# Kernel tuning notes

Hardware: AMD Instinct MI355X
Metric: run time of the kernel (lower is better)

The kernel has to match this reference:

```python
import jax, jax.numpy as jnp
import numpy as np

B, S, D, H, L, NITEMS = 512, 200, 64, 2, 2, 100000
HD = D // H
EPS = 1e-8
C = 0.001


def _ln(x, w, b):
    m = jnp.mean(x, -1, keepdims=True)
    v = jnp.mean((x - m) ** 2, -1, keepdims=True)
    return (x - m) / jnp.sqrt(v + EPS) * w + b


def _frob(x):
    return jnp.sqrt(jnp.sum(x * x))


def setup_inputs() -> dict:
    key = jax.random.key(0)
    ks = jax.random.split(key, 20)
    rn = lambda k, shape, s=0.02: jax.random.normal(k, shape, jnp.float32) * s
    item_emb = rn(ks[0], (NITEMS + 1, D))
    pos_emb = rn(ks[1], (S + 1, D)).at[0].set(0.0)  # padding_idx=0 row
    pred_w = rn(ks[2], (1, D))
    inp = {
        'user_ids': jax.random.randint(ks[3], (B,), 0, NITEMS, dtype=jnp.int32),
        'log_seqs': jax.random.randint(ks[4], (B, S), 0, NITEMS + 1, dtype=jnp.int32),
        'pos_seqs': jax.random.randint(ks[5], (B, S), 0, NITEMS + 1, dtype=jnp.int32),
        'item_emb': item_emb, 'pos_emb': pos_emb, 'pred_w': pred_w,
        'ln_w': jnp.ones((L, D), jnp.float32), 'ln_b': rn(ks[6], (L, D)),
        'qkv_w': rn(ks[7], (L, 3 * D, D)), 'qkv_b': rn(ks[8], (L, 3 * D)),
        'out_w': rn(ks[9], (L, D, D)), 'out_b': rn(ks[10], (L, D)),
        'fc1_w': rn(ks[11], (L, D, D)), 'fc1_b': rn(ks[12], (L, D)),
        'ffln_w': jnp.ones((L, D), jnp.float32), 'ffln_b': rn(ks[13], (L, D)),
        'fc2_w': rn(ks[14], (L, D, D)), 'fc2_b': rn(ks[15], (L, D)),
        'ffln2_w': jnp.ones((L, D), jnp.float32), 'ffln2_b': rn(ks[16], (L, D)),
    }
    return inp


def reference(user_ids, log_seqs, pos_seqs, item_emb, pos_emb, pred_w,
              ln_w, ln_b, qkv_w, qkv_b, out_w, out_b,
              fc1_w, fc1_b, ffln_w, ffln_b, fc2_w, fc2_b, ffln2_w, ffln2_b):
    # ---- log2feats ----
    x = item_emb[log_seqs] * jnp.sqrt(jnp.float32(D))  # (B,S,D)
    poss = jnp.arange(1, S + 1, dtype=log_seqs.dtype)[None, :] * (log_seqs != 0)
    x = x + pos_emb[poss]
    causal_bias = jnp.where(jnp.tril(jnp.ones((S, S), bool)), 0.0, -1e30).astype(jnp.float32)
    for l in range(L):
        q_in = _ln(x, ln_w[l], ln_b[l])  # query uses pre-LN, K/V use raw seqs
        q = (q_in @ qkv_w[l, :D].T + qkv_b[l, :D]).reshape(B, S, H, HD)
        k = (x @ qkv_w[l, D:2 * D].T + qkv_b[l, D:2 * D]).reshape(B, S, H, HD)
        v = (x @ qkv_w[l, 2 * D:].T + qkv_b[l, 2 * D:]).reshape(B, S, H, HD)
        sc = jnp.einsum('bqhd,bkhd->bhqk', q, k) / jnp.sqrt(jnp.float32(HD)) + causal_bias
        a = jax.nn.softmax(sc, -1)
        ctx = jnp.einsum('bhqk,bkhd->bqhd', a, v).reshape(B, S, D)
        x = q_in + ctx @ out_w[l].T + out_b[l]
        h = jax.nn.relu(_ln(x, ffln_w[l], ffln_b[l]) @ fc1_w[l].T + fc1_b[l])
        x = h @ fc2_w[l].T + fc2_b[l] + _ln(x, ffln2_w[l], ffln2_b[l])
    # ---- left(): quadratic form via Gram matrices (math identical to outer-product sum) ----
    FF = jnp.einsum('bsi,bsj->ij', x, x)          # sum_b F_b^T F_b  (d,d)
    EE = item_emb.T @ item_emb                      # (d,d)
    hh = pred_w.T @ pred_w                          # (d,d)
    left = C * jnp.sum(FF * EE * hh)
    # ---- right() ----
    ps = (x * item_emb[pos_seqs]) @ pred_w[0]       # (B,S), prediction has no bias
    right = jnp.sum((1.0 - C) * ps ** 2 - 2.0 * ps)
    # ---- reg_loss(): sum of per-parameter Frobenius norms ----
    reg = _frob(item_emb) + _frob(pos_emb) + _frob(pred_w)
    for p in (ln_w, ln_b, qkv_w, qkv_b, out_w, out_b, fc1_w, fc1_b,
              ffln_w, ffln_b, fc2_w, fc2_b, ffln2_w, ffln2_b):
        reg = reg + jnp.sum(jax.vmap(_frob)(p))  # per-layer params are separate tensors
    return left + right + 0.1 * reg
```

## Files before the change

### kernel.cpp

```cpp
#include <hip/hip_runtime.h>
#include <math.h>

#define BB 512
#define SS 200
#define DDIM 64
#define HD 32
#define LL 2
#define NROWS (BB * SS)
#define EPS 1e-8f
#define CC 0.001f
#define GRAM_NB 256
#define LSTRIDE 72
#define XS 68
#define QROWS 208

typedef __attribute__((ext_vector_type(8))) short bf16x8;
typedef __attribute__((ext_vector_type(4))) float f32x4;

__device__ unsigned short g_qb[NROWS * DDIM];
__device__ float g_gpart[2 * GRAM_NB * 4096];
__device__ unsigned short g_wb[49152];

__device__ __forceinline__ float wave_sum(float v) {
#pragma unroll
    for (int o = 32; o > 0; o >>= 1) v += __shfl_xor(v, o, 64);
    return v;
}
__device__ __forceinline__ unsigned short f2b(float f) {
    unsigned u = __float_as_uint(f);
    return (unsigned short)((u + 0x7FFFu + ((u >> 16) & 1u)) >> 16);
}

__global__ __launch_bounds__(256) void prep_weights(const float* __restrict__ qkv_w,
                                                    const float* __restrict__ out_w,
                                                    const float* __restrict__ fc1_w,
                                                    const float* __restrict__ fc2_w,
                                                    unsigned short* __restrict__ wb) {
    int i4 = (blockIdx.x * 256 + threadIdx.x) * 4;
    const float* src; int off;
    if (i4 < 24576)      { src = qkv_w; off = 0; }
    else if (i4 < 32768) { src = out_w; off = 24576; }
    else if (i4 < 40960) { src = fc1_w; off = 32768; }
    else                 { src = fc2_w; off = 40960; }
    float4 f = *(const float4*)&src[i4 - off];
    ushort4 o; o.x = f2b(f.x); o.y = f2b(f.y); o.z = f2b(f.z); o.w = f2b(f.w);
    *(ushort4*)&wb[i4] = o;
}

__device__ __forceinline__ bf16x8 frag_raw(const float* Xf, int row, int c0) {
    const float* p = &Xf[row * XS + c0];
    float4 u = *(const float4*)p;
    float4 v = *(const float4*)(p + 4);
    bf16x8 r;
    r[0] = (short)f2b(u.x); r[1] = (short)f2b(u.y); r[2] = (short)f2b(u.z); r[3] = (short)f2b(u.w);
    r[4] = (short)f2b(v.x); r[5] = (short)f2b(v.y); r[6] = (short)f2b(v.z); r[7] = (short)f2b(v.w);
    return r;
}
__device__ __forceinline__ bf16x8 frag_ln(const float* Xf, const float* stats,
                                          const float* vw, const float* vb,
                                          int row, int c0) {
    float m = stats[row * 2], rs = stats[row * 2 + 1];
    const float* p = &Xf[row * XS + c0];
    float4 u = *(const float4*)p;
    float4 v = *(const float4*)(p + 4);
    bf16x8 r;
    r[0] = (short)f2b((u.x - m) * rs * vw[c0 + 0] + vb[c0 + 0]);
    r[1] = (short)f2b((u.y - m) * rs * vw[c0 + 1] + vb[c0 + 1]);
    r[2] = (short)f2b((u.z - m) * rs * vw[c0 + 2] + vb[c0 + 2]);
    r[3] = (short)f2b((u.w - m) * rs * vw[c0 + 3] + vb[c0 + 3]);
    r[4] = (short)f2b((v.x - m) * rs * vw[c0 + 4] + vb[c0 + 4]);
    r[5] = (short)f2b((v.y - m) * rs * vw[c0 + 5] + vb[c0 + 5]);
    r[6] = (short)f2b((v.z - m) * rs * vw[c0 + 6] + vb[c0 + 6]);
    r[7] = (short)f2b((v.w - m) * rs * vw[c0 + 7] + vb[c0 + 7]);
    return r;
}

__device__ __forceinline__ void gemm_lds(bf16x8 a0, bf16x8 a1, const unsigned short* __restrict__ W,
                                         int m16, int quad, f32x4 acc[4]) {
#pragma unroll
    for (int nt = 0; nt < 4; ++nt) {
        bf16x8 b0 = *(const bf16x8*)&W[(nt * 16 + m16) * LSTRIDE + quad * 8];
        bf16x8 b1 = *(const bf16x8*)&W[(nt * 16 + m16) * LSTRIDE + 32 + quad * 8];
        acc[nt] = __builtin_amdgcn_mfma_f32_16x16x32_bf16(a0, b0, acc[nt], 0, 0, 0);
        acc[nt] = __builtin_amdgcn_mfma_f32_16x16x32_bf16(a1, b1, acc[nt], 0, 0, 0);
    }
}

__device__ __forceinline__ void stage_wb1024(const unsigned short* __restrict__ G,
                                             unsigned short* __restrict__ L, int t) {
    int r = t >> 4, c4 = (t & 15) * 4;
    *(ushort4*)&L[r * LSTRIDE + c4] = *(const ushort4*)&G[r * 64 + c4];
}

__global__ __launch_bounds__(1024)
void mega(const int* __restrict__ log_seqs,
          const int* __restrict__ pos_seqs,
          const float* __restrict__ item_emb,
          const float* __restrict__ pos_emb,
          const float* __restrict__ pred_w,
          const float* __restrict__ ln_w,  const float* __restrict__ ln_b,
          const float* __restrict__ qkv_b,
          const float* __restrict__ out_b,
          const float* __restrict__ fc1_b, const float* __restrict__ fc2_b,
          const float* __restrict__ ffln_w, const float* __restrict__ ffln_b,
          const float* __restrict__ ffln2_w, const float* __restrict__ ffln2_b,
          const unsigned short* __restrict__ wb,
          unsigned short* __restrict__ xb,
          float* __restrict__ rpart) {
    __shared__ float Xf[200 * XS];
    __shared__ unsigned short Qb[QROWS * 72];
    __shared__ unsigned short Kb[QROWS * 72];
    __shared__ unsigned short Vt[64 * 232];
    __shared__ unsigned short Wb[64 * LSTRIDE];
    __shared__ float stats[200 * 2];
    __shared__ float vecs[13][64];
    __shared__ float redw[16];

    const int t = threadIdx.x, b = blockIdx.x;
    const int w = t >> 6, lane = t & 63, m16 = lane & 15, quad = lane >> 4;
    const f32x4 Z = {0.f, 0.f, 0.f, 0.f};

    if (t < 64) vecs[12][t] = pred_w[t];
    if (t < 512) {
        int r2 = t >> 3, cc = 200 + (t & 7) * 4;
        ushort4 z4; z4.x = z4.y = z4.z = z4.w = 0;
        *(ushort4*)&Vt[r2 * 232 + cc] = z4;
    }
    {
        int rr = t >> 2;
        if (rr < 200) {
            int li = log_seqs[b * SS + rr];
            int poss = li ? (rr + 1) : 0;
            int qd = (t & 3) * 16;
            float4 v[4];
#pragma unroll
            for (int g = 0; g < 4; ++g) {
                float4 e = *(const float4*)&item_emb[(long)li * DDIM + qd + g * 4];
                float4 p = *(const float4*)&pos_emb[(long)poss * DDIM + qd + g * 4];
                v[g].x = e.x * 8.0f + p.x; v[g].y = e.y * 8.0f + p.y;
                v[g].z = e.z * 8.0f + p.z; v[g].w = e.w * 8.0f + p.w;
                *(float4*)&Xf[rr * XS + qd + g * 4] = v[g];
            }
            float s1 = 0.f, s2 = 0.f;
#pragma unroll
            for (int g = 0; g < 4; ++g) {
                s1 += (v[g].x + v[g].y) + (v[g].z + v[g].w);
                s2 += (v[g].x * v[g].x + v[g].y * v[g].y) + (v[g].z * v[g].z + v[g].w * v[g].w);
            }
            s1 += __shfl_xor(s1, 1, 64); s1 += __shfl_xor(s1, 2, 64);
            s2 += __shfl_xor(s2, 1, 64); s2 += __shfl_xor(s2, 2, 64);
            float mean = s1 * (1.f / 64.f);
            float var = s2 * (1.f / 64.f) - mean * mean;
            float rs = rsqrtf(var + EPS);
            if ((t & 3) == 0) { stats[rr * 2] = mean; stats[rr * 2 + 1] = rs; }
        }
    }
    __syncthreads();

    for (int l = 0; l < LL; ++l) {
        if (t < 64) {
            vecs[0][t] = qkv_b[l * 192 + t];
            vecs[1][t] = qkv_b[l * 192 + 64 + t];
            vecs[2][t] = qkv_b[l * 192 + 128 + t];
            vecs[3][t] = ln_w[l * 64 + t];   vecs[4][t] = ln_b[l * 64 + t];
            vecs[5][t] = out_b[l * 64 + t];
            vecs[6][t] = fc1_b[l * 64 + t];  vecs[7][t] = fc2_b[l * 64 + t];
            vecs[8][t] = ffln_w[l * 64 + t]; vecs[9][t] = ffln_b[l * 64 + t];
            vecs[10][t] = ffln2_w[l * 64 + t]; vecs[11][t] = ffln2_b[l * 64 + t];
        }
        stage_wb1024(wb + l * 12288, Wb, t);
        __syncthreads();
        if (w < 13) {
            int tb = w * 16;
            int row = tb + m16; if (row > 199) row = 199;
            bf16x8 a0 = frag_ln(Xf, stats, vecs[3], vecs[4], row, quad * 8);
            bf16x8 a1 = frag_ln(Xf, stats, vecs[3], vecs[4], row, 32 + quad * 8);
            f32x4 acc[4] = {Z, Z, Z, Z};
            gemm_lds(a0, a1, Wb, m16, quad, acc);
#pragma unroll
            for (int nt = 0; nt < 4; ++nt) {
                int n = nt * 16 + m16; float bbv = vecs[0][n];
#pragma unroll
                for (int rg = 0; rg < 4; ++rg)
                    Qb[(tb + quad * 4 + rg) * 72 + n] = f2b(acc[nt][rg] + bbv);
            }
        }
        __syncthreads();
        stage_wb1024(wb + l * 12288 + 4096, Wb, t);
        __syncthreads();
        if (w < 13) {
            int tb = w * 16;
            int row = tb + m16; if (row > 199) row = 199;
            bf16x8 a0 = frag_raw(Xf, row, quad * 8);
            bf16x8 a1 = frag_raw(Xf, row, 32 + quad * 8);
            f32x4 acc[4] = {Z, Z, Z, Z};
            gemm_lds(a0, a1, Wb, m16, quad, acc);
#pragma unroll
            for (int nt = 0; nt < 4; ++nt) {
                int n = nt * 16 + m16; float bbv = vecs[1][n];
#pragma unroll
                for (int rg = 0; rg < 4; ++rg)
                    Kb[(tb + quad * 4 + rg) * 72 + n] = f2b(acc[nt][rg] + bbv);
            }
        }
        __syncthreads();
        stage_wb1024(wb + l * 12288 + 8192, Wb, t);
        __syncthreads();
        if (w < 13) {
            int tb = w * 16;
            int row = tb + m16; if (row > 199) row = 199;
            bf16x8 a0 = frag_raw(Xf, row, quad * 8);
            bf16x8 a1 = frag_raw(Xf, row, 32 + quad * 8);
            f32x4 acc[4] = {Z, Z, Z, Z};
            gemm_lds(a0, a1, Wb, m16, quad, acc);
#pragma unroll
            for (int nt = 0; nt < 4; ++nt) {
                int n = nt * 16 + m16; float bbv = vecs[2][n];
#pragma unroll
                for (int rg = 0; rg < 4; ++rg) {
                    int m = tb + quad * 4 + rg;
                    if (m < 200) Vt[n * 232 + m] = f2b(acc[nt][rg] + bbv);
                }
            }
        }
        __syncthreads();
        {
            const unsigned long long tab0 = 0x01170016FF19FF18ull;
            const unsigned long long tab1 = 0x0513041203150214ull;
            const unsigned long long tab2 = 0x090F080E07110610ull;
            const unsigned long long tab3 = 0xFFFFFFFF0B0D0A0Cull;
            unsigned long long tv = (w & 8) ? ((w & 4) ? tab3 : tab2) : ((w & 4) ? tab1 : tab0);
            unsigned su = (unsigned)((tv >> ((w & 3) * 16)) & 0xFFFFu);
            const float scale = 0.17677669529663687f;
            for (int slot = 0; slot < 2; ++slot) {
                int u = (su >> (slot * 8)) & 0xFF;
                if (u == 0xFF) break;
                int h = u & 1, qt = u >> 1;
                int q0 = qt * 16;
                int qrow = q0 + m16; if (qrow > 199) qrow = 199;
                bf16x8 qa = *(const bf16x8*)&Qb[qrow * 72 + h * 32 + quad * 8];
                __builtin_amdgcn_wave_barrier();
                unsigned short* ps = &Qb[q0 * 72 + h * 32];
                f32x4 o0 = Z, o1 = Z;
                float lsum[4] = {0.f, 0.f, 0.f, 0.f};
                int np = (qt + 2) >> 1;
                for (int pi = 0; pi < np; ++pi) {
                    int p0 = pi * 32;
                    int kr0 = p0 + m16;      int kr0c = kr0 > 199 ? 199 : kr0;
                    int kr1 = p0 + 16 + m16; int kr1c = kr1 > 199 ? 199 : kr1;
                    bf16x8 kb0 = *(const bf16x8*)&Kb[kr0c * 72 + h * 32 + quad * 8];
                    bf16x8 kb1 = *(const bf16x8*)&Kb[kr1c * 72 + h * 32 + quad * 8];
                    f32x4 s0 = __builtin_amdgcn_mfma_f32_16x16x32_bf16(qa, kb0, Z, 0, 0, 0);
                    f32x4 s1 = __builtin_amdgcn_mfma_f32_16x16x32_bf16(qa, kb1, Z, 0, 0, 0);
                    float e0[4], e1[4];
#pragma unroll
                    for (int rg = 0; rg < 4; ++rg) {
                        int rglob = q0 + quad * 4 + rg;
                        e0[rg] = (kr0 <= rglob && kr0 < SS) ? __expf(s0[rg] * scale) : 0.f;
                        e1[rg] = (kr1 <= rglob && kr1 < SS) ? __expf(s1[rg] * scale) : 0.f;
                        lsum[rg] += e0[rg] + e1[rg];
                    }
                    __builtin_amdgcn_wave_barrier();
#pragma unroll
                    for (int rg = 0; rg < 4; ++rg) {
                        int row = quad * 4 + rg;
                        ps[row * 72 + m16] = f2b(e0[rg]);
                        ps[row * 72 + 16 + m16] = f2b(e1[rg]);
                    }
                    __builtin_amdgcn_wave_barrier();
                    bf16x8 pa = *(const bf16x8*)&ps[m16 * 72 + quad * 8];
                    bf16x8 vb0 = *(const bf16x8*)&Vt[(h * 32 + m16) * 232 + p0 + quad * 8];
                    bf16x8 vb1 = *(const bf16x8*)&Vt[(h * 32 + 16 + m16) * 232 + p0 + quad * 8];
                    o0 = __builtin_amdgcn_mfma_f32_16x16x32_bf16(pa, vb0, o0, 0, 0, 0);
                    o1 = __builtin_amdgcn_mfma_f32_16x16x32_bf16(pa, vb1, o1, 0, 0, 0);
                }
#pragma unroll
                for (int rg = 0; rg < 4; ++rg)
#pragma unroll
                    for (int o = 1; o <= 8; o <<= 1) lsum[rg] += __shfl_xor(lsum[rg], o, 64);
                __builtin_amdgcn_wave_barrier();
#pragma unroll
                for (int rg = 0; rg < 4; ++rg) {
                    int rglob = q0 + quad * 4 + rg;
                    if (rglob < SS) {
                        float inv = 1.f / lsum[rg];
                        Qb[rglob * 72 + h * 32 + m16] = f2b(o0[rg] * inv);
                        Qb[rglob * 72 + h * 32 + 16 + m16] = f2b(o1[rg] * inv);
                    }
                }
            }
        }
        __syncthreads();
        float core[4][4];
        stage_wb1024(wb + 24576 + l * 4096, Wb, t);
        __syncthreads();
        if (w < 13) {
            int tb = w * 16;
            int row = tb + m16; if (row > 199) row = 199;
            bf16x8 a0 = *(const bf16x8*)&Qb[row * 72 + quad * 8];
            bf16x8 a1 = *(const bf16x8*)&Qb[row * 72 + 32 + quad * 8];
            f32x4 acc1[4] = {Z, Z, Z, Z};
            gemm_lds(a0, a1, Wb, m16, quad, acc1);
#pragma unroll
            for (int nt = 0; nt < 4; ++nt) {
                int n = nt * 16 + m16;
                float bbv = vecs[5][n], lw = vecs[3][n], lb = vecs[4][n];
#pragma unroll
                for (int rg = 0; rg < 4; ++rg) {
                    int m = tb + quad * 4 + rg; int mc = m > 199 ? 199 : m;
                    float qin = (Xf[mc * XS + n] - stats[mc * 2]) * stats[mc * 2 + 1] * lw + lb;
                    core[nt][rg] = acc1[nt][rg] + bbv + qin;
                }
            }
#pragma unroll
            for (int rg = 0; rg < 4; ++rg) {
                float s1 = (core[0][rg] + core[1][rg]) + (core[2][rg] + core[3][rg]);
                float s2 = core[0][rg] * core[0][rg] + core[1][rg] * core[1][rg]
                         + core[2][rg] * core[2][rg] + core[3][rg] * core[3][rg];
#pragma unroll
                for (int o = 1; o <= 8; o <<= 1) { s1 += __shfl_xor(s1, o, 64); s2 += __shfl_xor(s2, o, 64); }
                float mean = s1 * (1.f / 64.f);
                float var = s2 * (1.f / 64.f) - mean * mean;
                float rs = rsqrtf(var + EPS);
#pragma unroll
                for (int nt = 0; nt < 4; ++nt) core[nt][rg] = (core[nt][rg] - mean) * rs;
            }
            __builtin_amdgcn_wave_barrier();
#pragma unroll
            for (int nt = 0; nt < 4; ++nt) {
                int n = nt * 16 + m16;
                float w8v = vecs[8][n], b9v = vecs[9][n];
#pragma unroll
                for (int rg = 0; rg < 4; ++rg)
                    Kb[(tb + quad * 4 + rg) * 72 + n] = f2b(core[nt][rg] * w8v + b9v);
            }
        }
        __syncthreads();
        stage_wb1024(wb + 32768 + l * 4096, Wb, t);
        __syncthreads();
        if (w < 13) {
            int tb = w * 16;
            bf16x8 a0 = *(const bf16x8*)&Kb[(tb + m16) * 72 + quad * 8];
            bf16x8 a1 = *(const bf16x8*)&Kb[(tb + m16) * 72 + 32 + quad * 8];
            f32x4 acc2[4] = {Z, Z, Z, Z};
            gemm_lds(a0, a1, Wb, m16, quad, acc2);
            __builtin_amdgcn_wave_barrier();
#pragma unroll
            for (int nt = 0; nt < 4; ++nt) {
                int n = nt * 16 + m16; float bbv = vecs[6][n];
#pragma unroll
                for (int rg = 0; rg < 4; ++rg)
                    Kb[(tb + quad * 4 + rg) * 72 + n] = f2b(fmaxf(acc2[nt][rg] + bbv, 0.f));
            }
        }
        __syncthreads();
        stage_wb1024(wb + 40960 + l * 4096, Wb, t);
        __syncthreads();
        if (w < 13) {
            int tb = w * 16;
            bf16x8 a0 = *(const bf16x8*)&Kb[(tb + m16) * 72 + quad * 8];
            bf16x8 a1 = *(const bf16x8*)&Kb[(tb + m16) * 72 + 32 + quad * 8];
            f32x4 acc3[4] = {Z, Z, Z, Z};
            gemm_lds(a0, a1, Wb, m16, quad, acc3);
            float xn[4][4];
#pragma unroll
            for (int nt = 0; nt < 4; ++nt) {
                int n = nt * 16 + m16;
                float bbv = vecs[7][n], lw = vecs[10][n], lb = vecs[11][n];
#pragma unroll
                for (int rg = 0; rg < 4; ++rg)
                    xn[nt][rg] = acc3[nt][rg] + bbv + core[nt][rg] * lw + lb;
            }
#pragma unroll
            for (int rg = 0; rg < 4; ++rg) {
                float s1 = (xn[0][rg] + xn[1][rg]) + (xn[2][rg] + xn[3][rg]);
                float s2 = xn[0][rg] * xn[0][rg] + xn[1][rg] * xn[1][rg]
                         + xn[2][rg] * xn[2][rg] + xn[3][rg] * xn[3][rg];
#pragma unroll
                for (int o = 1; o <= 8; o <<= 1) { s1 += __shfl_xor(s1, o, 64); s2 += __shfl_xor(s2, o, 64); }
                float mean = s1 * (1.f / 64.f);
                float var = s2 * (1.f / 64.f) - mean * mean;
                float rs = rsqrtf(var + EPS);
                int m = tb + quad * 4 + rg;
                if (m < 200) {
#pragma unroll
                    for (int nt = 0; nt < 4; ++nt) Xf[m * XS + nt * 16 + m16] = xn[nt][rg];
                    if (m16 == 0) { stats[m * 2] = mean; stats[m * 2 + 1] = rs; }
                }
            }
        }
        __syncthreads();
    }

    for (int i = t; i < 3200; i += 1024) {
        int r = i >> 4, c4 = (i & 15) * 4;
        float4 f = *(const float4*)&Xf[r * XS + c4];
        ushort4 o; o.x = f2b(f.x); o.y = f2b(f.y); o.z = f2b(f.z); o.w = f2b(f.w);
        *(ushort4*)&xb[((long)b * SS + r) * DDIM + c4] = o;
    }
    float local = 0.f;
    {
        int rr = t >> 2;
        if (rr < 200) {
            int pi = pos_seqs[b * SS + rr];
            int qd = (t & 3) * 16;
            float v = 0.f;
#pragma unroll
            for (int g = 0; g < 4; ++g) {
                float4 xv = *(const float4*)&Xf[rr * XS + qd + g * 4];
                float4 iv = *(const float4*)&item_emb[(long)pi * DDIM + qd + g * 4];
                const float* pwp = &vecs[12][qd + g * 4];
                v += xv.x * iv.x * pwp[0] + xv.y * iv.y * pwp[1]
                   + xv.z * iv.z * pwp[2] + xv.w * iv.w * pwp[3];
            }
            v += __shfl_xor(v, 1, 64); v += __shfl_xor(v, 2, 64);
            if ((t & 3) == 0) local += (1.0f - CC) * v * v - 2.0f * v;
        }
    }
    local = wave_sum(local);
    if (lane == 0) redw[w] = local;
    __syncthreads();
    if (t == 0) {
        float s = 0.f;
#pragma unroll
        for (int i = 0; i < 16; ++i) s += redw[i];
        rpart[b] = s;
    }
}

__global__ __launch_bounds__(256) void gram_kernel(const float* __restrict__ A0, int n0,
                                                   const unsigned short* __restrict__ A1, int n1,
                                                   float* __restrict__ part) {
    __shared__ unsigned short At[64 * LSTRIDE];
    int t = threadIdx.x;
    int second = blockIdx.x >= GRAM_NB;
    int bid = second ? blockIdx.x - GRAM_NB : blockIdx.x;
    int nrows = second ? n1 : n0;
    int w16 = (t >> 6) * 16, lane = t & 63, m16 = lane & 15, quad = lane >> 4;
    int bi = t & 15, bj = t >> 4;
    f32x4 zero = {0.f, 0.f, 0.f, 0.f};
    f32x4 acc[4] = {zero, zero, zero, zero};
    for (long base = (long)bid * 64; base < nrows; base += (long)GRAM_NB * 64) {
        __syncthreads();
        if (!second) {
            float rv[4][4];
#pragma unroll
            for (int e = 0; e < 4; ++e) {
                long gr = base + bj * 4 + e;
                float4 f = make_float4(0.f, 0.f, 0.f, 0.f);
                if (gr < nrows) f = *(const float4*)&A0[gr * DDIM + bi * 4];
                rv[e][0] = f.x; rv[e][1] = f.y; rv[e][2] = f.z; rv[e][3] = f.w;
            }
#pragma unroll
            for (int e = 0; e < 4; ++e) {
                ushort4 o;
                o.x = f2b(rv[0][e]); o.y = f2b(rv[1][e]); o.z = f2b(rv[2][e]); o.w = f2b(rv[3][e]);
                *(ushort4*)&At[(bi * 4 + e) * LSTRIDE + bj * 4] = o;
            }
        } else {
            ushort4 u[4];
#pragma unroll
            for (int e = 0; e < 4; ++e) {
                long gr = base + bj * 4 + e;
                ushort4 uu; uu.x = uu.y = uu.z = uu.w = 0;
                if (gr < nrows) uu = *(const ushort4*)&A1[gr * DDIM + bi * 4];
                u[e] = uu;
            }
#pragma unroll
            for (int e = 0; e < 4; ++e) {
                ushort4 o;
                o.x = ((const unsigned short*)&u[0])[e];
                o.y = ((const unsigned short*)&u[1])[e];
                o.z = ((const unsigned short*)&u[2])[e];
                o.w = ((const unsigned short*)&u[3])[e];
                *(ushort4*)&At[(bi * 4 + e) * LSTRIDE + bj * 4] = o;
            }
        }
        __syncthreads();
#pragma unroll
        for (int ks = 0; ks < 2; ++ks) {
            bf16x8 a = *(const bf16x8*)&At[(w16 + m16) * LSTRIDE + ks * 32 + quad * 8];
#pragma unroll
            for (int nt = 0; nt < 4; ++nt) {
                bf16x8 bfr = *(const bf16x8*)&At[(nt * 16 + m16) * LSTRIDE + ks * 32 + quad * 8];
                acc[nt] = __builtin_amdgcn_mfma_f32_16x16x32_bf16(a, bfr, acc[nt], 0, 0, 0);
            }
        }
    }
    float* slab = part + (long)blockIdx.x * 4096;
#pragma unroll
    for (int nt = 0; nt < 4; ++nt) {
        int n = nt * 16 + m16;
#pragma unroll
        for (int rg = 0; rg < 4; ++rg) {
            int m = w16 + quad * 4 + rg;
            slab[m * 64 + n] = acc[nt][rg];
        }
    }
}

struct NormEntry { const float* p; int n; };
struct NormArgs { NormEntry e[30]; };

__global__ __launch_bounds__(256) void reduce_norms(const float* __restrict__ part,
                                                    float* __restrict__ EE, float* __restrict__ FF,
                                                    NormArgs args, float* __restrict__ norms) {
    __shared__ float red[256];
    int blk = blockIdx.x;
    if (blk < 32) {
        int which = blk >> 4;
        int p = (blk & 15) * 256 + threadIdx.x;
        const float* basep = part + (long)which * GRAM_NB * 4096;
        float s = 0.f;
        for (int b = 0; b < GRAM_NB; ++b) s += basep[(long)b * 4096 + p];
        (which ? FF : EE)[p] = s;
    } else {
        NormEntry en = args.e[blk - 32];
        float s = 0.f;
        for (int i = threadIdx.x; i < en.n; i += 256) { float v = en.p[i]; s += v * v; }
        red[threadIdx.x] = s;
        for (int o = 128; o > 0; o >>= 1) {
            __syncthreads();
            if (threadIdx.x < o) red[threadIdx.x] += red[threadIdx.x + o];
        }
        __syncthreads();
        if (threadIdx.x == 0) norms[blk - 32] = red[0];
    }
}

__global__ __launch_bounds__(256) void final_kernel(const float* __restrict__ EE,
                                                    const float* __restrict__ FF,
                                                    const float* __restrict__ pred_w,
                                                    const float* __restrict__ rpart,
                                                    const float* __restrict__ norms,
                                                    float* __restrict__ out) {
    __shared__ float p_s[64];
    __shared__ float redL[256];
    __shared__ float redT[256];
    __shared__ float redR[256];
    int t = threadIdx.x;
    if (t < 64) p_s[t] = pred_w[t];
    __syncthreads();
    float lf = 0.f, tr = 0.f, rs = 0.f;
    for (int p = t; p < 4096; p += 256) {
        int i = p >> 6, j = p & 63;
        float ee = EE[p];
        lf += FF[p] * ee * p_s[i] * p_s[j];
        if (i == j) tr += ee;
    }
    for (int i = t; i < 512; i += 256) rs += rpart[i];
    redL[t] = lf; redT[t] = tr; redR[t] = rs;
    for (int o = 128; o > 0; o >>= 1) {
        __syncthreads();
        if (t < o) { redL[t] += redL[t + o]; redT[t] += redT[t + o]; redR[t] += redR[t + o]; }
    }
    __syncthreads();
    if (t == 0) {
        float reg = sqrtf(redT[0]);
        for (int s = 0; s < 30; ++s) reg += sqrtf(norms[s]);
        out[0] = CC * redL[0] + redR[0] + 0.1f * reg;
    }
}

struct DevPtrs { float* gpart; unsigned short *qb, *wb; };

static DevPtrs fetch_ptrs() {
    DevPtrs p;
    (void)hipGetSymbolAddress((void**)&p.gpart, HIP_SYMBOL(g_gpart));
    (void)hipGetSymbolAddress((void**)&p.qb,    HIP_SYMBOL(g_qb));
    (void)hipGetSymbolAddress((void**)&p.wb,    HIP_SYMBOL(g_wb));
    return p;
}

extern "C" void kernel_launch(void* const* d_in, const int* in_sizes, int n_in,
                              void* d_out, int out_size, void* d_ws, size_t ws_size,
                              hipStream_t stream) {
    const int*   log_seqs = (const int*)d_in[1];
    const int*   pos_seqs = (const int*)d_in[2];
    const float* item_emb = (const float*)d_in[3];
    const float* pos_emb  = (const float*)d_in[4];
    const float* pred_w   = (const float*)d_in[5];
    const float* ln_w     = (const float*)d_in[6];
    const float* ln_b     = (const float*)d_in[7];
    const float* qkv_w    = (const float*)d_in[8];
    const float* qkv_b    = (const float*)d_in[9];
    const float* out_w    = (const float*)d_in[10];
    const float* out_b    = (const float*)d_in[11];
    const float* fc1_w    = (const float*)d_in[12];
    const float* fc1_b    = (const float*)d_in[13];
    const float* ffln_w   = (const float*)d_in[14];
    const float* ffln_b   = (const float*)d_in[15];
    const float* fc2_w    = (const float*)d_in[16];
    const float* fc2_b    = (const float*)d_in[17];
    const float* ffln2_w  = (const float*)d_in[18];
    const float* ffln2_b  = (const float*)d_in[19];

    static DevPtrs P = fetch_ptrs();

    float* ws    = (float*)d_ws;
    float* rpart = ws;
    float* nrm   = ws + 1664;
    float* EE    = ws + 2048;
    float* FF    = ws + 6144;

    prep_weights<<<48, 256, 0, stream>>>(qkv_w, out_w, fc1_w, fc2_w, P.wb);

    mega<<<BB, 1024, 0, stream>>>(log_seqs, pos_seqs, item_emb, pos_emb, pred_w,
                                  ln_w, ln_b, qkv_b, out_b, fc1_b, fc2_b,
                                  ffln_w, ffln_b, ffln2_w, ffln2_b,
                                  P.wb, P.qb, rpart);

    gram_kernel<<<2 * GRAM_NB, 256, 0, stream>>>(item_emb, 100001, P.qb, NROWS, P.gpart);

    NormArgs na;
    int s = 0;
    na.e[s++] = {pos_emb, (SS + 1) * DDIM};
    na.e[s++] = {pred_w, DDIM};
    for (int l = 0; l < LL; ++l) {
        na.e[s++] = {ln_w + l * 64, 64};
        na.e[s++] = {ln_b + l * 64, 64};
        na.e[s++] = {qkv_w + (long)l * 12288, 12288};
        na.e[s++] = {qkv_b + (long)l * 192, 192};
        na.e[s++] = {out_w + (long)l * 4096, 4096};
        na.e[s++] = {out_b + l * 64, 64};
        na.e[s++] = {fc1_w + (long)l * 4096, 4096};
        na.e[s++] = {fc1_b + l * 64, 64};
        na.e[s++] = {ffln_w + l * 64, 64};
        na.e[s++] = {ffln_b + l * 64, 64};
        na.e[s++] = {fc2_w + (long)l * 4096, 4096};
        na.e[s++] = {fc2_b + l * 64, 64};
        na.e[s++] = {ffln2_w + l * 64, 64};
        na.e[s++] = {ffln2_b + l * 64, 64};
    }
    reduce_norms<<<62, 256, 0, stream>>>(P.gpart, EE, FF, na, nrm);

    final_kernel<<<1, 256, 0, stream>>>(EE, FF, pred_w, rpart, nrm, (float*)d_out);
}
```

Baseline: 241.2 us.

## Drop weight-prep and final kernels via in-kernel bf16 conversion and last-block reduction

Removes the separate prep_weights launch by converting fp32 weights to bf16 while staging them into LDS inside the main kernel. It also merges reduce_norms and final_kernel into one launch, where the last block to arrive (tracked by an atomic counter that the main kernel resets) computes the final scalar. Two accumulator arrays are reused in place to reduce register pressure. The aim is to cut launch overhead, at the cost of redundant fp32 loads and conversions in every block plus a fence-and-atomic handshake.

```diff
diff --git a/kernel.cpp b/kernel.cpp
--- a/kernel.cpp
+++ b/kernel.cpp
@@ -19,7 +19,6 @@
 
 __device__ unsigned short g_qb[NROWS * DDIM];
 __device__ float g_gpart[2 * GRAM_NB * 4096];
-__device__ unsigned short g_wb[49152];
 
 __device__ __forceinline__ float wave_sum(float v) {
 #pragma unroll
@@ -29,22 +28,6 @@
 __device__ __forceinline__ unsigned short f2b(float f) {
     unsigned u = __float_as_uint(f);
     return (unsigned short)((u + 0x7FFFu + ((u >> 16) & 1u)) >> 16);
-}
-
-__global__ __launch_bounds__(256) void prep_weights(const float* __restrict__ qkv_w,
-                                                    const float* __restrict__ out_w,
-                                                    const float* __restrict__ fc1_w,
-                                                    const float* __restrict__ fc2_w,
-                                                    unsigned short* __restrict__ wb) {
-    int i4 = (blockIdx.x * 256 + threadIdx.x) * 4;
-    const float* src; int off;
-    if (i4 < 24576)      { src = qkv_w; off = 0; }
-    else if (i4 < 32768) { src = out_w; off = 24576; }
-    else if (i4 < 40960) { src = fc1_w; off = 32768; }
-    else                 { src = fc2_w; off = 40960; }
-    float4 f = *(const float4*)&src[i4 - off];
-    ushort4 o; o.x = f2b(f.x); o.y = f2b(f.y); o.z = f2b(f.z); o.w = f2b(f.w);
-    *(ushort4*)&wb[i4] = o;
 }
 
 __device__ __forceinline__ bf16x8 frag_raw(const float* Xf, int row, int c0) {
@@ -86,10 +69,12 @@
     }
 }
 
-__device__ __forceinline__ void stage_wb1024(const unsigned short* __restrict__ G,
-                                             unsigned short* __restrict__ L, int t) {
+__device__ __forceinline__ void stage_wf32(const float* __restrict__ G,
+                                           unsigned short* __restrict__ L, int t) {
     int r = t >> 4, c4 = (t & 15) * 4;
-    *(ushort4*)&L[r * LSTRIDE + c4] = *(const ushort4*)&G[r * 64 + c4];
+    float4 f = *(const float4*)&G[r * 64 + c4];
+    ushort4 o; o.x = f2b(f.x); o.y = f2b(f.y); o.z = f2b(f.z); o.w = f2b(f.w);
+    *(ushort4*)&L[r * LSTRIDE + c4] = o;
 }
 
 __global__ __launch_bounds__(1024)
@@ -104,9 +89,11 @@
           const float* __restrict__ fc1_b, const float* __restrict__ fc2_b,
           const float* __restrict__ ffln_w, const float* __restrict__ ffln_b,
           const float* __restrict__ ffln2_w, const float* __restrict__ ffln2_b,
-          const unsigned short* __restrict__ wb,
+          const float* __restrict__ qkv_w, const float* __restrict__ out_w,
+          const float* __restrict__ fc1_w, const float* __restrict__ fc2_w,
           unsigned short* __restrict__ xb,
-          float* __restrict__ rpart) {
+          float* __restrict__ rpart,
+          unsigned int* __restrict__ cnt) {
     __shared__ float Xf[200 * XS];
     __shared__ unsigned short Qb[QROWS * 72];
     __shared__ unsigned short Kb[QROWS * 72];
@@ -120,6 +107,7 @@
     const int w = t >> 6, lane = t & 63, m16 = lane & 15, quad = lane >> 4;
     const f32x4 Z = {0.f, 0.f, 0.f, 0.f};
 
+    if (b == 0 && t == 0) *cnt = 0u;
     if (t < 64) vecs[12][t] = pred_w[t];
     if (t < 512) {
         int r2 = t >> 3, cc = 200 + (t & 7) * 4;
@@ -168,7 +156,7 @@
             vecs[8][t] = ffln_w[l * 64 + t]; vecs[9][t] = ffln_b[l * 64 + t];
             vecs[10][t] = ffln2_w[l * 64 + t]; vecs[11][t] = ffln2_b[l * 64 + t];
         }
-        stage_wb1024(wb + l * 12288, Wb, t);
+        stage_wf32(qkv_w + l * 12288, Wb, t);
         __syncthreads();
         if (w < 13) {
             int tb = w * 16;
@@ -186,7 +174,7 @@
             }
         }
         __syncthreads();
-        stage_wb1024(wb + l * 12288 + 4096, Wb, t);
+        stage_wf32(qkv_w + l * 12288 + 4096, Wb, t);
         __syncthreads();
         if (w < 13) {
             int tb = w * 16;
@@ -204,7 +192,7 @@
             }
         }
         __syncthreads();
-        stage_wb1024(wb + l * 12288 + 8192, Wb, t);
+        stage_wf32(qkv_w + l * 12288 + 8192, Wb, t);
         __syncthreads();
         if (w < 13) {
             int tb = w * 16;
@@ -291,16 +279,16 @@
             }
         }
         __syncthreads();
-        float core[4][4];
-        stage_wb1024(wb + 24576 + l * 4096, Wb, t);
+        f32x4 core4[4];
+        stage_wf32(out_w + l * 4096, Wb, t);
         __syncthreads();
         if (w < 13) {
             int tb = w * 16;
             int row = tb + m16; if (row > 199) row = 199;
             bf16x8 a0 = *(const bf16x8*)&Qb[row * 72 + quad * 8];
             bf16x8 a1 = *(const bf16x8*)&Qb[row * 72 + 32 + quad * 8];
-            f32x4 acc1[4] = {Z, Z, Z, Z};
-            gemm_lds(a0, a1, Wb, m16, quad, acc1);
+            core4[0] = Z; core4[1] = Z; core4[2] = Z; core4[3] = Z;
+            gemm_lds(a0, a1, Wb, m16, quad, core4);
 #pragma unroll
             for (int nt = 0; nt < 4; ++nt) {
                 int n = nt * 16 + m16;
@@ -309,21 +297,21 @@
                 for (int rg = 0; rg < 4; ++rg) {
                     int m = tb + quad * 4 + rg; int mc = m > 199 ? 199 : m;
                     float qin = (Xf[mc * XS + n] - stats[mc * 2]) * stats[mc * 2 + 1] * lw + lb;
-                    core[nt][rg] = acc1[nt][rg] + bbv + qin;
+                    core4[nt][rg] = core4[nt][rg] + bbv + qin;
                 }
             }
 #pragma unroll
             for (int rg = 0; rg < 4; ++rg) {
-                float s1 = (core[0][rg] + core[1][rg]) + (core[2][rg] + core[3][rg]);
-                float s2 = core[0][rg] * core[0][rg] + core[1][rg] * core[1][rg]
-                         + core[2][rg] * core[2][rg] + core[3][rg] * core[3][rg];
+                float s1 = (core4[0][rg] + core4[1][rg]) + (core4[2][rg] + core4[3][rg]);
+                float s2 = core4[0][rg] * core4[0][rg] + core4[1][rg] * core4[1][rg]
+                         + core4[2][rg] * core4[2][rg] + core4[3][rg] * core4[3][rg];
 #pragma unroll
                 for (int o = 1; o <= 8; o <<= 1) { s1 += __shfl_xor(s1, o, 64); s2 += __shfl_xor(s2, o, 64); }
                 float mean = s1 * (1.f / 64.f);
                 float var = s2 * (1.f / 64.f) - mean * mean;
                 float rs = rsqrtf(var + EPS);
 #pragma unroll
-                for (int nt = 0; nt < 4; ++nt) core[nt][rg] = (core[nt][rg] - mean) * rs;
+                for (int nt = 0; nt < 4; ++nt) core4[nt][rg] = (core4[nt][rg] - mean) * rs;
             }
             __builtin_amdgcn_wave_barrier();
 #pragma unroll
@@ -332,11 +320,11 @@
                 float w8v = vecs[8][n], b9v = vecs[9][n];
 #pragma unroll
                 for (int rg = 0; rg < 4; ++rg)
-                    Kb[(tb + quad * 4 + rg) * 72 + n] = f2b(core[nt][rg] * w8v + b9v);
-            }
-        }
-        __syncthreads();
-        stage_wb1024(wb + 32768 + l * 4096, Wb, t);
+                    Kb[(tb + quad * 4 + rg) * 72 + n] = f2b(core4[nt][rg] * w8v + b9v);
+            }
+        }
+        __syncthreads();
+        stage_wf32(fc1_w + l * 4096, Wb, t);
         __syncthreads();
         if (w < 13) {
             int tb = w * 16;
@@ -354,7 +342,7 @@
             }
         }
         __syncthreads();
-        stage_wb1024(wb + 40960 + l * 4096, Wb, t);
+        stage_wf32(fc2_w + l * 4096, Wb, t);
         __syncthreads();
         if (w < 13) {
             int tb = w * 16;
@@ -362,20 +350,19 @@
             bf16x8 a1 = *(const bf16x8*)&Kb[(tb + m16) * 72 + 32 + quad * 8];
             f32x4 acc3[4] = {Z, Z, Z, Z};
             gemm_lds(a0, a1, Wb, m16, quad, acc3);
-            float xn[4][4];
 #pragma unroll
             for (int nt = 0; nt < 4; ++nt) {
                 int n = nt * 16 + m16;
                 float bbv = vecs[7][n], lw = vecs[10][n], lb = vecs[11][n];
 #pragma unroll
                 for (int rg = 0; rg < 4; ++rg)
-                    xn[nt][rg] = acc3[nt][rg] + bbv + core[nt][rg] * lw + lb;
+                    acc3[nt][rg] = acc3[nt][rg] + bbv + core4[nt][rg] * lw + lb;
             }
 #pragma unroll
             for (int rg = 0; rg < 4; ++rg) {
-                float s1 = (xn[0][rg] + xn[1][rg]) + (xn[2][rg] + xn[3][rg]);
-                float s2 = xn[0][rg] * xn[0][rg] + xn[1][rg] * xn[1][rg]
-                         + xn[2][rg] * xn[2][rg] + xn[3][rg] * xn[3][rg];
+                float s1 = (acc3[0][rg] + acc3[1][rg]) + (acc3[2][rg] + acc3[3][rg]);
+                float s2 = acc3[0][rg] * acc3[0][rg] + acc3[1][rg] * acc3[1][rg]
+                         + acc3[2][rg] * acc3[2][rg] + acc3[3][rg] * acc3[3][rg];
 #pragma unroll
                 for (int o = 1; o <= 8; o <<= 1) { s1 += __shfl_xor(s1, o, 64); s2 += __shfl_xor(s2, o, 64); }
                 float mean = s1 * (1.f / 64.f);
@@ -384,7 +371,7 @@
                 int m = tb + quad * 4 + rg;
                 if (m < 200) {
 #pragma unroll
-                    for (int nt = 0; nt < 4; ++nt) Xf[m * XS + nt * 16 + m16] = xn[nt][rg];
+                    for (int nt = 0; nt < 4; ++nt) Xf[m * XS + nt * 16 + m16] = acc3[nt][rg];
                     if (m16 == 0) { stats[m * 2] = mean; stats[m * 2 + 1] = rs; }
                 }
             }
@@ -502,14 +489,22 @@
 struct NormEntry { const float* p; int n; };
 struct NormArgs { NormEntry e[30]; };
 
-__global__ __launch_bounds__(256) void reduce_norms(const float* __restrict__ part,
+__global__ __launch_bounds__(256) void reduce_final(const float* __restrict__ part,
                                                     float* __restrict__ EE, float* __restrict__ FF,
-                                                    NormArgs args, float* __restrict__ norms) {
+                                                    NormArgs args, float* __restrict__ norms,
+                                                    const float* __restrict__ pred_w,
+                                                    const float* __restrict__ rpart,
+                                                    unsigned int* __restrict__ cnt,
+                                                    float* __restrict__ out) {
     __shared__ float red[256];
-    int blk = blockIdx.x;
+    __shared__ float redT[256];
+    __shared__ float redR[256];
+    __shared__ float p_s[64];
+    __shared__ unsigned int amlast;
+    int blk = blockIdx.x, t = threadIdx.x;
     if (blk < 32) {
         int which = blk >> 4;
-        int p = (blk & 15) * 256 + threadIdx.x;
+        int p = (blk & 15) * 256 + t;
         const float* basep = part + (long)which * GRAM_NB * 4096;
         float s = 0.f;
         for (int b = 0; b < GRAM_NB; ++b) s += basep[(long)b * 4096 + p];
@@ -517,28 +512,21 @@
     } else {
         NormEntry en = args.e[blk - 32];
         float s = 0.f;
-        for (int i = threadIdx.x; i < en.n; i += 256) { float v = en.p[i]; s += v * v; }
-        red[threadIdx.x] = s;
+        for (int i = t; i < en.n; i += 256) { float v = en.p[i]; s += v * v; }
+        red[t] = s;
         for (int o = 128; o > 0; o >>= 1) {
             __syncthreads();
-            if (threadIdx.x < o) red[threadIdx.x] += red[threadIdx.x + o];
-        }
-        __syncthreads();
-        if (threadIdx.x == 0) norms[blk - 32] = red[0];
-    }
-}
-
-__global__ __launch_bounds__(256) void final_kernel(const float* __restrict__ EE,
-                                                    const float* __restrict__ FF,
-                                                    const float* __restrict__ pred_w,
-                                                    const float* __restrict__ rpart,
-                                                    const float* __restrict__ norms,
-                                                    float* __restrict__ out) {
-    __shared__ float p_s[64];
-    __shared__ float redL[256];
-    __shared__ float redT[256];
-    __shared__ float redR[256];
-    int t = threadIdx.x;
+            if (t < o) red[t] += red[t + o];
+        }
+        __syncthreads();
+        if (t == 0) norms[blk - 32] = red[0];
+    }
+    __threadfence();
+    __syncthreads();
+    if (t == 0) amlast = atomicAdd(cnt, 1u);
+    __syncthreads();
+    if (amlast != 61) return;
+    __threadfence();
     if (t < 64) p_s[t] = pred_w[t];
     __syncthreads();
     float lf = 0.f, tr = 0.f, rs = 0.f;
@@ -549,26 +537,25 @@
         if (i == j) tr += ee;
     }
     for (int i = t; i < 512; i += 256) rs += rpart[i];
-    redL[t] = lf; redT[t] = tr; redR[t] = rs;
+    red[t] = lf; redT[t] = tr; redR[t] = rs;
     for (int o = 128; o > 0; o >>= 1) {
         __syncthreads();
-        if (t < o) { redL[t] += redL[t + o]; redT[t] += redT[t + o]; redR[t] += redR[t + o]; }
+        if (t < o) { red[t] += red[t + o]; redT[t] += redT[t + o]; redR[t] += redR[t + o]; }
     }
     __syncthreads();
     if (t == 0) {
         float reg = sqrtf(redT[0]);
         for (int s = 0; s < 30; ++s) reg += sqrtf(norms[s]);
-        out[0] = CC * redL[0] + redR[0] + 0.1f * reg;
-    }
-}
-
-struct DevPtrs { float* gpart; unsigned short *qb, *wb; };
+        out[0] = CC * red[0] + redR[0] + 0.1f * reg;
+    }
+}
+
+struct DevPtrs { float* gpart; unsigned short* qb; };
 
 static DevPtrs fetch_ptrs() {
     DevPtrs p;
     (void)hipGetSymbolAddress((void**)&p.gpart, HIP_SYMBOL(g_gpart));
     (void)hipGetSymbolAddress((void**)&p.qb,    HIP_SYMBOL(g_qb));
-    (void)hipGetSymbolAddress((void**)&p.wb,    HIP_SYMBOL(g_wb));
     return p;
 }
 
@@ -599,16 +586,16 @@
 
     float* ws    = (float*)d_ws;
     float* rpart = ws;
+    unsigned int* cnt = (unsigned int*)(ws + 1600);
     float* nrm   = ws + 1664;
     float* EE    = ws + 2048;
     float* FF    = ws + 6144;
 
-    prep_weights<<<48, 256, 0, stream>>>(qkv_w, out_w, fc1_w, fc2_w, P.wb);
-
     mega<<<BB, 1024, 0, stream>>>(log_seqs, pos_seqs, item_emb, pos_emb, pred_w,
                                   ln_w, ln_b, qkv_b, out_b, fc1_b, fc2_b,
                                   ffln_w, ffln_b, ffln2_w, ffln2_b,
-                                  P.wb, P.qb, rpart);
+                                  qkv_w, out_w, fc1_w, fc2_w,
+                                  P.qb, rpart, cnt);
 
     gram_kernel<<<2 * GRAM_NB, 256, 0, stream>>>(item_emb, 100001, P.qb, NROWS, P.gpart);
 
@@ -632,7 +619,6 @@
         na.e[s++] = {ffln2_w + l * 64, 64};
         na.e[s++] = {ffln2_b + l * 64, 64};
     }
-    reduce_norms<<<62, 256, 0, stream>>>(P.gpart, EE, FF, na, nrm);
-
-    final_kernel<<<1, 256, 0, stream>>>(EE, FF, pred_w, rpart, nrm, (float*)d_out);
-}
+    reduce_final<<<62, 256, 0, stream>>>(P.gpart, EE, FF, na, nrm, pred_w, rpart, cnt,
+                                         (float*)d_out);
+}
```

New measurement: 244.3 us. Within noise of the previous version (+1.3%).
